# Performance work log

Measured on AMD Instinct MI355X. Metric: run time of the kernel, lower is better.

Reference implementation:

```python
import jax, jax.numpy as jnp
import numpy as np

N_ENT = 500000
N_REL = 1000
EMB = 256
B = 65536
EPS = 1e-12


def setup_inputs() -> dict:
    key = jax.random.key(0)
    ks = jax.random.split(key, 7)
    all_emb = jax.random.normal(ks[0], (N_ENT + N_REL, EMB), dtype=jnp.float32)
    pos_h = jax.random.randint(ks[1], (B,), 0, N_ENT)
    pos_r = jax.random.randint(ks[2], (B,), 0, N_REL)
    pos_t = jax.random.randint(ks[3], (B,), 0, N_ENT)
    neg_h = jax.random.randint(ks[4], (B,), 0, N_ENT)
    neg_r = jax.random.randint(ks[5], (B,), 0, N_REL)
    neg_t = jax.random.randint(ks[6], (B,), 0, N_ENT)
    return {"all_emb": all_emb, "pos_h": pos_h, "pos_r": pos_r, "pos_t": pos_t,
            "neg_h": neg_h, "neg_r": neg_r, "neg_t": neg_t, "n_ent": N_ENT}


def reference(all_emb, pos_h, pos_r, pos_t, neg_h, neg_r, neg_t, n_ent):
    # forward() first L2-normalizes entity rows in-place (normalize_entity_weights)
    ent = all_emb[:n_ent]
    nrm = jnp.maximum(jnp.linalg.norm(ent, axis=1, keepdims=True), EPS)
    emb = jnp.concatenate([ent / nrm, all_emb[n_ent:]], axis=0)

    # sparse.mm(adj, emb) with rows (+1@h, +1@(n_ent+r), -1@t) == gather-combine
    def score(h, r, t):
        v = emb[h] + emb[r + n_ent] - emb[t]          # [B, EMB]
        return -jnp.sum(v * v, axis=1)                 # -||.||_2^2, [B]

    pos_calc = score(pos_h, pos_r, pos_t)
    neg_calc = score(neg_h, neg_r, neg_t)
    return (pos_calc, neg_calc)
```

## Files before the change

### kernel.cpp

```cpp
#include <hip/hip_runtime.h>


#define EMB 256
#define EPS 1e-12f

#define NRM_RPW 4

__global__ __launch_bounds__(256) void inv_norm_kernel(
    const float* __restrict__ emb, float* __restrict__ inv_norm,
    const int* __restrict__ n_ent_ptr)
{
    const int wave = (blockIdx.x * blockDim.x + threadIdx.x) >> 6;
    const int lane = threadIdx.x & 63;
    const int n_ent = *n_ent_ptr;
    const int base = wave * NRM_RPW;
    if (base >= n_ent) return;

    float s[NRM_RPW];
#pragma unroll
    for (int i = 0; i < NRM_RPW; ++i) {
        const int row = base + i;
        float4 v = make_float4(0.f, 0.f, 0.f, 0.f);
        if (row < n_ent)
            v = ((const float4*)(emb + (size_t)row * EMB))[lane];
        s[i] = v.x * v.x + v.y * v.y + v.z * v.z + v.w * v.w;
    }
#pragma unroll
    for (int d = 32; d >= 1; d >>= 1)
#pragma unroll
        for (int i = 0; i < NRM_RPW; ++i)
            s[i] += __shfl_xor(s[i], d, 64);

    if (lane == 0) {
        const float4 o = make_float4(
            1.0f / fmaxf(sqrtf(s[0]), EPS),
            1.0f / fmaxf(sqrtf(s[1]), EPS),
            1.0f / fmaxf(sqrtf(s[2]), EPS),
            1.0f / fmaxf(sqrtf(s[3]), EPS));
        if (base + NRM_RPW <= n_ent) {
            *(float4*)(inv_norm + base) = o;
        } else {
            inv_norm[base] = o.x;
            if (base + 1 < n_ent) inv_norm[base + 1] = o.y;
            if (base + 2 < n_ent) inv_norm[base + 2] = o.z;
        }
    }
}

#define SPW 4
#define WPB 4

__global__ __launch_bounds__(256, 5) void transe_score_lds_kernel(
    const float* __restrict__ emb,
    const float* __restrict__ inv_norm,
    const int* __restrict__ pos_h, const int* __restrict__ pos_r, const int* __restrict__ pos_t,
    const int* __restrict__ neg_h, const int* __restrict__ neg_r, const int* __restrict__ neg_t,
    const int* __restrict__ n_ent_ptr,
    float* __restrict__ out, int B)
{
    __shared__ float lds[WPB * 2 * SPW * EMB];

    const int wave = (blockIdx.x * blockDim.x + threadIdx.x) >> 6;
    const int lane = threadIdx.x & 63;
    const int wib  = threadIdx.x >> 6;
    const int base = wave * SPW;
    if (base >= 2 * B) return;

    const int n_ent = *n_ent_ptr;

    const int* __restrict__ hsrc;
    const int* __restrict__ rsrc;
    const int* __restrict__ tsrc;
    int off;
    if (base < B) { hsrc = pos_h; rsrc = pos_r; tsrc = pos_t; off = base; }
    else          { hsrc = neg_h; rsrc = neg_r; tsrc = neg_t; off = base - B; }

    const int4 hh = *(const int4*)(hsrc + off);
    const int4 rr = *(const int4*)(rsrc + off);
    const int4 tt = *(const int4*)(tsrc + off);
    const int hi[SPW] = {hh.x, hh.y, hh.z, hh.w};
    const int ri[SPW] = {rr.x, rr.y, rr.z, rr.w};
    const int ti[SPW] = {tt.x, tt.y, tt.z, tt.w};

    float* wl = lds + wib * (2 * SPW * EMB);
#pragma unroll
    for (int s = 0; s < SPW; ++s) {
        const float* hg = emb + (size_t)hi[s] * EMB + lane * 4;
        const float* tg = emb + (size_t)ti[s] * EMB + lane * 4;
        __builtin_amdgcn_global_load_lds(hg, wl + s * EMB,         16, 0, 0);
        __builtin_amdgcn_global_load_lds(tg, wl + (SPW + s) * EMB, 16, 0, 0);
    }

    float4 rv[SPW];
    float inh[SPW], itn[SPW];
#pragma unroll
    for (int s = 0; s < SPW; ++s) {
        rv[s]  = ((const float4*)(emb + ((size_t)ri[s] + (size_t)n_ent) * EMB))[lane];
        inh[s] = inv_norm[hi[s]];
        itn[s] = inv_norm[ti[s]];
    }

    asm volatile("s_waitcnt vmcnt(0)" ::: "memory");
    __builtin_amdgcn_sched_barrier(0);

    float sq[SPW];
#pragma unroll
    for (int s = 0; s < SPW; ++s) {
        const float4 hv = ((const float4*)(wl + s * EMB))[lane];
        const float4 tv = ((const float4*)(wl + (SPW + s) * EMB))[lane];
        const float vx = hv.x * inh[s] + rv[s].x - tv.x * itn[s];
        const float vy = hv.y * inh[s] + rv[s].y - tv.y * itn[s];
        const float vz = hv.z * inh[s] + rv[s].z - tv.z * itn[s];
        const float vw = hv.w * inh[s] + rv[s].w - tv.w * itn[s];
        sq[s] = vx * vx + vy * vy + vz * vz + vw * vw;
    }
#pragma unroll
    for (int d = 32; d >= 1; d >>= 1)
#pragma unroll
        for (int k = 0; k < SPW; ++k)
            sq[k] += __shfl_xor(sq[k], d, 64);

    if (lane == 0)
        *(float4*)(out + base) = make_float4(-sq[0], -sq[1], -sq[2], -sq[3]);
}

__global__ __launch_bounds__(256) void transe_score_fused_kernel(
    const float* __restrict__ emb,
    const int* __restrict__ pos_h, const int* __restrict__ pos_r, const int* __restrict__ pos_t,
    const int* __restrict__ neg_h, const int* __restrict__ neg_r, const int* __restrict__ neg_t,
    const int* __restrict__ n_ent_ptr,
    float* __restrict__ out, int B)
{
    const int wave = (blockIdx.x * blockDim.x + threadIdx.x) >> 6;
    const int lane = threadIdx.x & 63;
    const int base = wave * SPW;
    if (base >= 2 * B) return;

    const int n_ent = *n_ent_ptr;

    const int* __restrict__ hsrc;
    const int* __restrict__ rsrc;
    const int* __restrict__ tsrc;
    int off;
    if (base < B) { hsrc = pos_h; rsrc = pos_r; tsrc = pos_t; off = base; }
    else          { hsrc = neg_h; rsrc = neg_r; tsrc = neg_t; off = base - B; }

    const int4 hh = *(const int4*)(hsrc + off);
    const int4 rr = *(const int4*)(rsrc + off);
    const int4 tt = *(const int4*)(tsrc + off);

    const int hi[SPW] = {hh.x, hh.y, hh.z, hh.w};
    const int ri[SPW] = {rr.x, rr.y, rr.z, rr.w};
    const int ti[SPW] = {tt.x, tt.y, tt.z, tt.w};

    float4 hv[SPW], tv[SPW], rv[SPW];
#pragma unroll
    for (int s = 0; s < SPW; ++s) {
        hv[s] = ((const float4*)(emb + (size_t)hi[s] * EMB))[lane];
        tv[s] = ((const float4*)(emb + (size_t)ti[s] * EMB))[lane];
        rv[s] = ((const float4*)(emb + ((size_t)ri[s] + (size_t)n_ent) * EMB))[lane];
    }

    float red[2 * SPW];
#pragma unroll
    for (int s = 0; s < SPW; ++s) {
        red[s]       = hv[s].x * hv[s].x + hv[s].y * hv[s].y + hv[s].z * hv[s].z + hv[s].w * hv[s].w;
        red[SPW + s] = tv[s].x * tv[s].x + tv[s].y * tv[s].y + tv[s].z * tv[s].z + tv[s].w * tv[s].w;
    }
#pragma unroll
    for (int d = 32; d >= 1; d >>= 1) {
#pragma unroll
        for (int k = 0; k < 2 * SPW; ++k)
            red[k] += __shfl_xor(red[k], d, 64);
    }

    float sq[SPW];
#pragma unroll
    for (int s = 0; s < SPW; ++s) {
        const float inh = 1.0f / fmaxf(sqrtf(red[s]), EPS);
        const float itn = 1.0f / fmaxf(sqrtf(red[SPW + s]), EPS);
        const float vx = hv[s].x * inh + rv[s].x - tv[s].x * itn;
        const float vy = hv[s].y * inh + rv[s].y - tv[s].y * itn;
        const float vz = hv[s].z * inh + rv[s].z - tv[s].z * itn;
        const float vw = hv[s].w * inh + rv[s].w - tv[s].w * itn;
        sq[s] = vx * vx + vy * vy + vz * vz + vw * vw;
    }
#pragma unroll
    for (int d = 32; d >= 1; d >>= 1) {
#pragma unroll
        for (int k = 0; k < SPW; ++k)
            sq[k] += __shfl_xor(sq[k], d, 64);
    }

    if (lane == 0)
        *(float4*)(out + base) = make_float4(-sq[0], -sq[1], -sq[2], -sq[3]);
}

extern "C" void kernel_launch(void* const* d_in, const int* in_sizes, int n_in,
                              void* d_out, int out_size, void* d_ws, size_t ws_size,
                              hipStream_t stream) {
    const float* emb  = (const float*)d_in[0];
    const int* pos_h  = (const int*)d_in[1];
    const int* pos_r  = (const int*)d_in[2];
    const int* pos_t  = (const int*)d_in[3];
    const int* neg_h  = (const int*)d_in[4];
    const int* neg_r  = (const int*)d_in[5];
    const int* neg_t  = (const int*)d_in[6];
    const int* n_ent  = (const int*)d_in[7];
    float* out = (float*)d_out;

    const int B = in_sizes[1];
    const int total = 2 * B;
    const size_t rows_total = (size_t)in_sizes[0] / EMB;

    const int waves_b = (total + SPW - 1) / SPW;
    const int grid_b  = (waves_b * 64 + 255) / 256;

    if (d_ws != nullptr && ws_size >= rows_total * sizeof(float)) {
        float* inv_norm = (float*)d_ws;

        const long long waves_a = ((long long)rows_total + NRM_RPW - 1) / NRM_RPW;
        const int grid_a = (int)((waves_a * 64 + 255) / 256);

        inv_norm_kernel<<<grid_a, 256, 0, stream>>>(emb, inv_norm, n_ent);
        transe_score_lds_kernel<<<grid_b, 256, 0, stream>>>(
            emb, inv_norm, pos_h, pos_r, pos_t, neg_h, neg_r, neg_t, n_ent, out, B);
    } else {
        transe_score_fused_kernel<<<grid_b, 256, 0, stream>>>(
            emb, pos_h, pos_r, pos_t, neg_h, neg_r, neg_t, n_ent, out, B);
    }
}
```

Baseline: 695.8 us.

## Materialize normalized entity table in fp16 and gather half-width rows

The normalization pre-pass now writes a full normalized entity table in fp16 instead of only per-row inverse norms. The scoring kernel then gathers 512-byte fp16 head and tail rows and drops the LDS async-load staging and the separate inverse-norm lookups. The aim is to halve the bytes of the random gather, which appears to be the costly part. In exchange the pre-pass writes a table of roughly 256 MB, the workspace must be much larger (otherwise the fused fallback kernel runs instead), and fp16 rounding adds some error to the normalized embeddings.

Result: slower. 718.3 us (+3.2%).

```diff
diff --git a/kernel.cpp b/kernel.cpp
--- a/kernel.cpp
+++ b/kernel.cpp
@@ -1,13 +1,16 @@
 #include <hip/hip_runtime.h>
+#include <hip/hip_fp16.h>
 
 
 #define EMB 256
 #define EPS 1e-12f
 
+typedef _Float16 half4 __attribute__((ext_vector_type(4)));
+
 #define NRM_RPW 4
 
-__global__ __launch_bounds__(256) void inv_norm_kernel(
-    const float* __restrict__ emb, float* __restrict__ inv_norm,
+__global__ __launch_bounds__(256) void normalize_f16_kernel(
+    const float* __restrict__ emb, _Float16* __restrict__ tab,
     const int* __restrict__ n_ent_ptr)
 {
     const int wave = (blockIdx.x * blockDim.x + threadIdx.x) >> 6;
@@ -16,14 +19,15 @@
     const int base = wave * NRM_RPW;
     if (base >= n_ent) return;
 
+    float4 v[NRM_RPW];
     float s[NRM_RPW];
 #pragma unroll
     for (int i = 0; i < NRM_RPW; ++i) {
         const int row = base + i;
-        float4 v = make_float4(0.f, 0.f, 0.f, 0.f);
+        v[i] = make_float4(0.f, 0.f, 0.f, 0.f);
         if (row < n_ent)
-            v = ((const float4*)(emb + (size_t)row * EMB))[lane];
-        s[i] = v.x * v.x + v.y * v.y + v.z * v.z + v.w * v.w;
+            v[i] = ((const float4*)(emb + (size_t)row * EMB))[lane];
+        s[i] = v[i].x * v[i].x + v[i].y * v[i].y + v[i].z * v[i].z + v[i].w * v[i].w;
     }
 #pragma unroll
     for (int d = 32; d >= 1; d >>= 1)
@@ -31,38 +35,33 @@
         for (int i = 0; i < NRM_RPW; ++i)
             s[i] += __shfl_xor(s[i], d, 64);
 
-    if (lane == 0) {
-        const float4 o = make_float4(
-            1.0f / fmaxf(sqrtf(s[0]), EPS),
-            1.0f / fmaxf(sqrtf(s[1]), EPS),
-            1.0f / fmaxf(sqrtf(s[2]), EPS),
-            1.0f / fmaxf(sqrtf(s[3]), EPS));
-        if (base + NRM_RPW <= n_ent) {
-            *(float4*)(inv_norm + base) = o;
-        } else {
-            inv_norm[base] = o.x;
-            if (base + 1 < n_ent) inv_norm[base + 1] = o.y;
-            if (base + 2 < n_ent) inv_norm[base + 2] = o.z;
+#pragma unroll
+    for (int i = 0; i < NRM_RPW; ++i) {
+        const int row = base + i;
+        if (row < n_ent) {
+            const float inv = 1.0f / fmaxf(sqrtf(s[i]), EPS);
+            half4 o;
+            o.x = (_Float16)(v[i].x * inv);
+            o.y = (_Float16)(v[i].y * inv);
+            o.z = (_Float16)(v[i].z * inv);
+            o.w = (_Float16)(v[i].w * inv);
+            ((half4*)(tab + (size_t)row * EMB))[lane] = o;
         }
     }
 }
 
 #define SPW 4
-#define WPB 4
-
-__global__ __launch_bounds__(256, 5) void transe_score_lds_kernel(
+
+__global__ __launch_bounds__(256) void transe_score_f16_kernel(
     const float* __restrict__ emb,
-    const float* __restrict__ inv_norm,
+    const _Float16* __restrict__ tab,
     const int* __restrict__ pos_h, const int* __restrict__ pos_r, const int* __restrict__ pos_t,
     const int* __restrict__ neg_h, const int* __restrict__ neg_r, const int* __restrict__ neg_t,
     const int* __restrict__ n_ent_ptr,
     float* __restrict__ out, int B)
 {
-    __shared__ float lds[WPB * 2 * SPW * EMB];
-
     const int wave = (blockIdx.x * blockDim.x + threadIdx.x) >> 6;
     const int lane = threadIdx.x & 63;
-    const int wib  = threadIdx.x >> 6;
     const int base = wave * SPW;
     if (base >= 2 * B) return;
 
@@ -78,40 +77,27 @@
     const int4 hh = *(const int4*)(hsrc + off);
     const int4 rr = *(const int4*)(rsrc + off);
     const int4 tt = *(const int4*)(tsrc + off);
+
     const int hi[SPW] = {hh.x, hh.y, hh.z, hh.w};
     const int ri[SPW] = {rr.x, rr.y, rr.z, rr.w};
     const int ti[SPW] = {tt.x, tt.y, tt.z, tt.w};
 
-    float* wl = lds + wib * (2 * SPW * EMB);
-#pragma unroll
-    for (int s = 0; s < SPW; ++s) {
-        const float* hg = emb + (size_t)hi[s] * EMB + lane * 4;
-        const float* tg = emb + (size_t)ti[s] * EMB + lane * 4;
-        __builtin_amdgcn_global_load_lds(hg, wl + s * EMB,         16, 0, 0);
-        __builtin_amdgcn_global_load_lds(tg, wl + (SPW + s) * EMB, 16, 0, 0);
-    }
-
+    half4  hv[SPW], tv[SPW];
     float4 rv[SPW];
-    float inh[SPW], itn[SPW];
-#pragma unroll
-    for (int s = 0; s < SPW; ++s) {
-        rv[s]  = ((const float4*)(emb + ((size_t)ri[s] + (size_t)n_ent) * EMB))[lane];
-        inh[s] = inv_norm[hi[s]];
-        itn[s] = inv_norm[ti[s]];
-    }
-
-    asm volatile("s_waitcnt vmcnt(0)" ::: "memory");
-    __builtin_amdgcn_sched_barrier(0);
+#pragma unroll
+    for (int s = 0; s < SPW; ++s) {
+        hv[s] = ((const half4*)(tab + (size_t)hi[s] * EMB))[lane];
+        tv[s] = ((const half4*)(tab + (size_t)ti[s] * EMB))[lane];
+        rv[s] = ((const float4*)(emb + ((size_t)ri[s] + (size_t)n_ent) * EMB))[lane];
+    }
 
     float sq[SPW];
 #pragma unroll
     for (int s = 0; s < SPW; ++s) {
-        const float4 hv = ((const float4*)(wl + s * EMB))[lane];
-        const float4 tv = ((const float4*)(wl + (SPW + s) * EMB))[lane];
-        const float vx = hv.x * inh[s] + rv[s].x - tv.x * itn[s];
-        const float vy = hv.y * inh[s] + rv[s].y - tv.y * itn[s];
-        const float vz = hv.z * inh[s] + rv[s].z - tv.z * itn[s];
-        const float vw = hv.w * inh[s] + rv[s].w - tv.w * itn[s];
+        const float vx = (float)hv[s].x + rv[s].x - (float)tv[s].x;
+        const float vy = (float)hv[s].y + rv[s].y - (float)tv[s].y;
+        const float vz = (float)hv[s].z + rv[s].z - (float)tv[s].z;
+        const float vw = (float)hv[s].w + rv[s].w - (float)tv[s].w;
         sq[s] = vx * vx + vy * vy + vz * vz + vw * vw;
     }
 #pragma unroll
@@ -216,15 +202,15 @@
     const int waves_b = (total + SPW - 1) / SPW;
     const int grid_b  = (waves_b * 64 + 255) / 256;
 
-    if (d_ws != nullptr && ws_size >= rows_total * sizeof(float)) {
-        float* inv_norm = (float*)d_ws;
+    if (d_ws != nullptr && ws_size >= rows_total * EMB * sizeof(_Float16)) {
+        _Float16* tab = (_Float16*)d_ws;
 
         const long long waves_a = ((long long)rows_total + NRM_RPW - 1) / NRM_RPW;
         const int grid_a = (int)((waves_a * 64 + 255) / 256);
 
-        inv_norm_kernel<<<grid_a, 256, 0, stream>>>(emb, inv_norm, n_ent);
-        transe_score_lds_kernel<<<grid_b, 256, 0, stream>>>(
-            emb, inv_norm, pos_h, pos_r, pos_t, neg_h, neg_r, neg_t, n_ent, out, B);
+        normalize_f16_kernel<<<grid_a, 256, 0, stream>>>(emb, tab, n_ent);
+        transe_score_f16_kernel<<<grid_b, 256, 0, stream>>>(
+            emb, tab, pos_h, pos_r, pos_t, neg_h, neg_r, neg_t, n_ent, out, B);
     } else {
         transe_score_fused_kernel<<<grid_b, 256, 0, stream>>>(
             emb, pos_h, pos_r, pos_t, neg_h, neg_r, neg_t, n_ent, out, B);
```
